# Kernel optimization log

Hardware: AMD Instinct MI355X
Metric: run time of the kernel (lower is better)

## Reference

```python
import jax, jax.numpy as jnp
import numpy as np

B, P, K, O = 16384, 64, 64, 64

def setup_inputs() -> dict:
    key = jax.random.key(0)
    k1, k2 = jax.random.split(key)
    x = jax.random.normal(k1, (B, P, K), dtype=jnp.float32)
    W = jax.random.normal(k2, (P, K, O), dtype=jnp.float32) * (1.0 / np.sqrt(K))
    bias = jnp.zeros((P, O), dtype=jnp.float32)
    return {"x": x, "W": W, "bias": bias}

def reference(x, W, bias):
    # Block-diagonal linear: per-part matmul fused into one batched einsum,
    # then bias add (channels_last over last dim) and relu activation.
    out = jnp.einsum('bpk,pko->bpo', x, W) + bias  # [B, P, O]
    return jax.nn.relu(out)
```

## Files before the change

### kernel.cpp

```cpp
#include <hip/hip_runtime.h>


#define KDIM   64
#define ODIM   64
#define PK     4096
#define CHUNK  64
#define NCHUNKS 4
#define ROWS_PER_BLOCK (CHUNK * NCHUNKS)
#define NBLOCKGROUPS (16384 / ROWS_PER_BLOCK)

typedef __attribute__((address_space(1))) const unsigned int gl_u32;
typedef __attribute__((address_space(3))) unsigned int lds_u32;

__global__ __launch_bounds__(256, 3) void parts_linear_relu(
    const float* __restrict__ x, const float* __restrict__ W,
    const float* __restrict__ bias, float* __restrict__ out)
{
  __shared__ float wbuf[KDIM * ODIM];
  __shared__ float xbuf[2][CHUNK * KDIM];

  const int tid  = threadIdx.x;
  const int wave = tid >> 6;
  const int lane = tid & 63;

  const int p  = blockIdx.x & 63;
  const int g  = blockIdx.x >> 6;
  const int b0 = g * ROWS_PER_BLOCK;

  {
    const float* Wp = W + p * (KDIM * ODIM);
    char* dst0 = (char*)wbuf + tid * 16;
#pragma unroll
    for (int i = 0; i < 4; ++i) {
      __builtin_amdgcn_global_load_lds(
          (gl_u32*)(Wp + i * 1024 + tid * 4),
          (lds_u32*)(dst0 + i * 4096), 16, 0, 0);
    }
  }

  auto stage = [&](int buf, int browbase) {
    const float* src0 = x + (browbase + (tid >> 4)) * PK + p * KDIM + ((tid & 15) << 2);
    char* dst0 = (char*)(&xbuf[buf][0]) + tid * 16;
#pragma unroll
    for (int i = 0; i < 4; ++i) {
      __builtin_amdgcn_global_load_lds(
          (gl_u32*)(src0 + i * 16 * PK),
          (lds_u32*)(dst0 + i * 4096), 16, 0, 0);
    }
  };

  stage(0, b0);

  const float bv = bias[p * ODIM + lane];

  for (int c = 0; c < NCHUNKS; ++c) {
    __syncthreads();
    if (c + 1 < NCHUNKS) stage((c + 1) & 1, b0 + (c + 1) * CHUNK);

    const float* xb = &xbuf[c & 1][wave * 16 * KDIM];

    float acc[16];
#pragma unroll
    for (int r = 0; r < 16; ++r) acc[r] = 0.f;

#pragma unroll 1
    for (int k4 = 0; k4 < KDIM / 4; ++k4) {
      const float w0 = wbuf[(4 * k4 + 0) * ODIM + lane];
      const float w1 = wbuf[(4 * k4 + 1) * ODIM + lane];
      const float w2 = wbuf[(4 * k4 + 2) * ODIM + lane];
      const float w3 = wbuf[(4 * k4 + 3) * ODIM + lane];
      const float* xk = xb + 4 * k4;
#pragma unroll
      for (int r = 0; r < 16; ++r) {
        const float4 xq = *reinterpret_cast<const float4*>(xk + r * KDIM);
        acc[r] = fmaf(xq.x, w0, acc[r]);
        acc[r] = fmaf(xq.y, w1, acc[r]);
        acc[r] = fmaf(xq.z, w2, acc[r]);
        acc[r] = fmaf(xq.w, w3, acc[r]);
      }
    }

    const int rowglob = b0 + c * CHUNK + wave * 16;
#pragma unroll
    for (int r = 0; r < 16; ++r) {
      const float v = fmaxf(acc[r] + bv, 0.0f);
      out[(rowglob + r) * PK + p * ODIM + lane] = v;
    }
  }
}

extern "C" void kernel_launch(void* const* d_in, const int* in_sizes, int n_in,
                              void* d_out, int out_size, void* d_ws, size_t ws_size,
                              hipStream_t stream) {
  const float* x    = (const float*)d_in[0];
  const float* W    = (const float*)d_in[1];
  const float* bias = (const float*)d_in[2];
  float* out        = (float*)d_out;

  dim3 grid(64 * NBLOCKGROUPS);
  parts_linear_relu<<<grid, 256, 0, stream>>>(x, W, bias, out);
}
```

Baseline: 501.9 us.

## Read x directly from global memory with uniform loads instead of LDS staging

Removes the double-buffered LDS staging of x and its per-chunk barriers. Each wave now loads its 16 rows of x straight from global memory with wave-uniform float4 loads, which may become scalar or broadcast loads. LDS use drops, so occupancy is raised to 4 blocks per SIMD group. The risk is that global-load latency is exposed inside the k loop without prefetching, and x reads become many small uniform accesses instead of coalesced bulk copies.

```diff
diff --git a/kernel.cpp b/kernel.cpp
--- a/kernel.cpp
+++ b/kernel.cpp
@@ -4,20 +4,19 @@
 #define KDIM   64
 #define ODIM   64
 #define PK     4096
-#define CHUNK  64
-#define NCHUNKS 4
-#define ROWS_PER_BLOCK (CHUNK * NCHUNKS)
+#define SLABROWS 16
+#define NSLABS 4
+#define ROWS_PER_BLOCK 256
 #define NBLOCKGROUPS (16384 / ROWS_PER_BLOCK)
 
 typedef __attribute__((address_space(1))) const unsigned int gl_u32;
 typedef __attribute__((address_space(3))) unsigned int lds_u32;
 
-__global__ __launch_bounds__(256, 3) void parts_linear_relu(
+__global__ __launch_bounds__(256, 4) void parts_linear_relu(
     const float* __restrict__ x, const float* __restrict__ W,
     const float* __restrict__ bias, float* __restrict__ out)
 {
   __shared__ float wbuf[KDIM * ODIM];
-  __shared__ float xbuf[2][CHUNK * KDIM];
 
   const int tid  = threadIdx.x;
   const int wave = tid >> 6;
@@ -37,31 +36,16 @@
           (lds_u32*)(dst0 + i * 4096), 16, 0, 0);
     }
   }
+  const float bv = bias[p * ODIM + lane];
+  __syncthreads();
 
-  auto stage = [&](int buf, int browbase) {
-    const float* src0 = x + (browbase + (tid >> 4)) * PK + p * KDIM + ((tid & 15) << 2);
-    char* dst0 = (char*)(&xbuf[buf][0]) + tid * 16;
+  for (int c = 0; c < NSLABS; ++c) {
+    const int row0 = b0 + c * 64 + wave * SLABROWS;
+    const float* xr0 = x + (size_t)row0 * PK + p * KDIM;
+
+    float acc[SLABROWS];
 #pragma unroll
-    for (int i = 0; i < 4; ++i) {
-      __builtin_amdgcn_global_load_lds(
-          (gl_u32*)(src0 + i * 16 * PK),
-          (lds_u32*)(dst0 + i * 4096), 16, 0, 0);
-    }
-  };
-
-  stage(0, b0);
-
-  const float bv = bias[p * ODIM + lane];
-
-  for (int c = 0; c < NCHUNKS; ++c) {
-    __syncthreads();
-    if (c + 1 < NCHUNKS) stage((c + 1) & 1, b0 + (c + 1) * CHUNK);
-
-    const float* xb = &xbuf[c & 1][wave * 16 * KDIM];
-
-    float acc[16];
-#pragma unroll
-    for (int r = 0; r < 16; ++r) acc[r] = 0.f;
+    for (int r = 0; r < SLABROWS; ++r) acc[r] = 0.f;
 
 #pragma unroll 1
     for (int k4 = 0; k4 < KDIM / 4; ++k4) {
@@ -69,22 +53,30 @@
       const float w1 = wbuf[(4 * k4 + 1) * ODIM + lane];
       const float w2 = wbuf[(4 * k4 + 2) * ODIM + lane];
       const float w3 = wbuf[(4 * k4 + 3) * ODIM + lane];
-      const float* xk = xb + 4 * k4;
+
 #pragma unroll
-      for (int r = 0; r < 16; ++r) {
-        const float4 xq = *reinterpret_cast<const float4*>(xk + r * KDIM);
-        acc[r] = fmaf(xq.x, w0, acc[r]);
-        acc[r] = fmaf(xq.y, w1, acc[r]);
-        acc[r] = fmaf(xq.z, w2, acc[r]);
-        acc[r] = fmaf(xq.w, w3, acc[r]);
+      for (int h = 0; h < 2; ++h) {
+        float4 xq[8];
+#pragma unroll
+        for (int r = 0; r < 8; ++r)
+          xq[r] = *reinterpret_cast<const float4*>(
+                      xr0 + (size_t)(h * 8 + r) * PK + 4 * k4);
+#pragma unroll
+        for (int r = 0; r < 8; ++r) {
+          float a = acc[h * 8 + r];
+          a = fmaf(xq[r].x, w0, a);
+          a = fmaf(xq[r].y, w1, a);
+          a = fmaf(xq[r].z, w2, a);
+          a = fmaf(xq[r].w, w3, a);
+          acc[h * 8 + r] = a;
+        }
       }
     }
 
-    const int rowglob = b0 + c * CHUNK + wave * 16;
+    float* o0 = out + (size_t)row0 * PK + p * ODIM + lane;
 #pragma unroll
-    for (int r = 0; r < 16; ++r) {
-      const float v = fmaxf(acc[r] + bv, 0.0f);
-      out[(rowglob + r) * PK + p * ODIM + lane] = v;
+    for (int r = 0; r < SLABROWS; ++r) {
+      o0[(size_t)r * PK] = fmaxf(acc[r] + bv, 0.0f);
     }
   }
 }
```

After: 867.6 us. +72.9%, slower.
